# Optimization experiments

Measured on AMD Instinct MI355X. Metric: run time of the kernel, lower is better.

Reference implementation:

```python
import jax, jax.numpy as jnp
import numpy as np

N_USER = 100000
N_ITEM = 50000
N = N_USER + N_ITEM
N_EDGES = 1200000
D = 64
NEG_SLOPE = 0.01  # torch leaky_relu default
EPS = 1e-12       # torch F.normalize default


def setup_inputs() -> dict:
    key = jax.random.key(0)
    ks = jax.random.split(key, 9)
    user_emb = jax.random.normal(ks[0], (N_USER, D), dtype=jnp.float32) * 0.1
    item_emb = jax.random.normal(ks[1], (N_ITEM, D), dtype=jnp.float32) * 0.1
    edge_row = jax.random.randint(ks[2], (N_EDGES,), 0, N, dtype=jnp.int32)
    edge_col = jax.random.randint(ks[3], (N_EDGES,), 0, N, dtype=jnp.int32)
    edge_val = jax.random.uniform(ks[4], (N_EDGES,), dtype=jnp.float32)
    Wf = jax.random.normal(ks[5], (3, D, D), dtype=jnp.float32) * (1.0 / np.sqrt(D))
    bf = jnp.zeros((3, D), dtype=jnp.float32)
    Wb = jax.random.normal(ks[6], (3, D, D), dtype=jnp.float32) * (1.0 / np.sqrt(D))
    bb = jnp.zeros((3, D), dtype=jnp.float32)
    return {"user_emb": user_emb, "item_emb": item_emb,
            "edge_row": edge_row, "edge_col": edge_col, "edge_val": edge_val,
            "Wf": Wf, "bf": bf, "Wb": Wb, "bb": bb}


def _spmm_plus_eye(edge_row, edge_col, edge_val, E):
    # (H + I) @ E : gather source features, scale, segment-sum into rows, add E
    msgs = edge_val[:, None] * E[edge_col]          # [n_edges, D]
    agg = jax.ops.segment_sum(msgs, edge_row, num_segments=N)
    return agg + E


def reference(user_emb, item_emb, edge_row, edge_col, edge_val, Wf, bf, Wb, bb):
    E_l = jnp.concatenate([user_emb, item_emb], axis=0)  # [N, D]
    all_emb = [E_l]
    for i in range(3):
        front = _spmm_plus_eye(edge_row, edge_col, edge_val, E_l)
        front_cal = jax.nn.leaky_relu(front @ Wf[i].T + bf[i], NEG_SLOPE)
        back = jax.nn.leaky_relu((E_l * front) @ Wb[i].T + bb[i], NEG_SLOPE)
        E_l = front_cal + back  # dropout p=0.5 treated as eval-mode identity
        norm = jnp.maximum(jnp.linalg.norm(E_l, axis=1, keepdims=True), EPS)
        all_emb.append(E_l / norm)
    all_emb = jnp.concatenate(all_emb, axis=1)  # [N, 4*D]
    return all_emb[:N_USER], all_emb[N_USER:]
```

## Files before the change

### kernel.cpp

```cpp
#include <hip/hip_runtime.h>
#include <hip/hip_bf16.h>
#include <stdint.h>

#define N_USER 100000
#define N_ITEM 50000
#define NTOT   150000
#define NEDGE  1200000
#define D      64
#define OUTD   256
#define NEG    0.01f
#define NBLK   586
#define WPLANE 1028

__global__ void k_init(const float* __restrict__ ue, const float* __restrict__ ie,
                       float* __restrict__ E, float* __restrict__ out) {
    int t = blockIdx.x * blockDim.x + threadIdx.x;
    if (t >= NTOT * 16) return;
    int r = t >> 4, q = t & 15;
    const float* src = (r < N_USER) ? (ue + (size_t)r * D)
                                    : (ie + (size_t)(r - N_USER) * D);
    float4 v = *(const float4*)(src + q * 4);
    *(float4*)(E + (size_t)r * D + q * 4) = v;
    *(float4*)(out + (size_t)r * OUTD + q * 4) = v;
}

__global__ void k_hist(const int* __restrict__ row, int* __restrict__ cnt) {
    int e = blockIdx.x * blockDim.x + threadIdx.x;
    if (e < NEDGE) atomicAdd(&cnt[row[e]], 1);
}

__global__ void k_scan_a(const int* __restrict__ cnt, int* __restrict__ part) {
    __shared__ int s[4];
    int i = blockIdx.x * 256 + threadIdx.x;
    int v = (i < NTOT) ? cnt[i] : 0;
    for (int off = 32; off; off >>= 1) v += __shfl_down(v, off, 64);
    if ((threadIdx.x & 63) == 0) s[threadIdx.x >> 6] = v;
    __syncthreads();
    if (threadIdx.x == 0) part[blockIdx.x] = s[0] + s[1] + s[2] + s[3];
}

__global__ void k_scan_b(int* __restrict__ part) {
    __shared__ int s[1024];
    int t = threadIdx.x;
    int v = (t < NBLK) ? part[t] : 0;
    s[t] = v;
    __syncthreads();
    for (int off = 1; off < 1024; off <<= 1) {
        int x = (t >= off) ? s[t - off] : 0;
        __syncthreads();
        s[t] += x;
        __syncthreads();
    }
    if (t < NBLK) part[t] = s[t] - v;
}

__global__ void k_scan_c(const int* __restrict__ cnt, const int* __restrict__ part,
                         int* __restrict__ offs, int* __restrict__ cur) {
    __shared__ int ws[4];
    int i = blockIdx.x * 256 + threadIdx.x;
    int v = (i < NTOT) ? cnt[i] : 0;
    int lane = threadIdx.x & 63, w = threadIdx.x >> 6;
    int x = v;
    for (int o = 1; o < 64; o <<= 1) {
        int y = __shfl_up(x, o, 64);
        if (lane >= o) x += y;
    }
    if (lane == 63) ws[w] = x;
    __syncthreads();
    int base = part[blockIdx.x];
    for (int k = 0; k < w; k++) base += ws[k];
    int excl = base + x - v;
    if (i < NTOT) { offs[i] = excl; cur[i] = excl; }
    if (i == 0) offs[NTOT] = NEDGE;
}

__global__ void k_scatter(const int* __restrict__ row, const int* __restrict__ col,
                          const float* __restrict__ val, int* __restrict__ cur,
                          int2* __restrict__ ce) {
    int e = blockIdx.x * blockDim.x + threadIdx.x;
    if (e >= NEDGE) return;
    int r = row[e];
    int p = atomicAdd(&cur[r], 1);
    int2 u;
    u.x = col[e];
    u.y = __float_as_int(val[e]);
    ce[p] = u;
}

__global__ void k_spmm(const float* __restrict__ E, const int* __restrict__ offs,
                       const int2* __restrict__ ce, float* __restrict__ front) {
    int r = blockIdx.x * (blockDim.x >> 6) + (threadIdx.x >> 6);
    int d = threadIdx.x & 63;
    if (r >= NTOT) return;
    int s = offs[r], e = offs[r + 1];
    float acc = E[(size_t)r * D + d];
    float a0 = 0.f, a1 = 0.f, a2 = 0.f, a3 = 0.f;
    int p = s;
    for (; p + 4 <= e; p += 4) {
        int2 c0 = ce[p + 0];
        int2 c1 = ce[p + 1];
        int2 c2 = ce[p + 2];
        int2 c3 = ce[p + 3];
        float x0 = E[(size_t)c0.x * D + d];
        float x1 = E[(size_t)c1.x * D + d];
        float x2 = E[(size_t)c2.x * D + d];
        float x3 = E[(size_t)c3.x * D + d];
        a0 = fmaf(__int_as_float(c0.y), x0, a0);
        a1 = fmaf(__int_as_float(c1.y), x1, a1);
        a2 = fmaf(__int_as_float(c2.y), x2, a2);
        a3 = fmaf(__int_as_float(c3.y), x3, a3);
    }
    for (; p < e; ++p) {
        int2 c = ce[p];
        acc = fmaf(__int_as_float(c.y), E[(size_t)c.x * D + d], acc);
    }
    acc += (a0 + a1) + (a2 + a3);
    front[(size_t)r * D + d] = acc;
}

__global__ __launch_bounds__(256) void k_rowmv(
    const float* __restrict__ front, float* __restrict__ E,
    const float* __restrict__ Wf, const float* __restrict__ bfv,
    const float* __restrict__ Wb, const float* __restrict__ bbv,
    float* __restrict__ out, int chunk) {
    __shared__ float wfs[4 * WPLANE];
    __shared__ float wbs[4 * WPLANE];
    {
        int t  = threadIdx.x;
        int j  = t >> 2;
        int kq = t & 3;
        const float* fsrc = Wf + (size_t)j * D + kq * 16;
        const float* bsrc = Wb + (size_t)j * D + kq * 16;
        float* fdst = wfs + kq * WPLANE + j * 16;
        float* bdst = wbs + kq * WPLANE + j * 16;
        #pragma unroll
        for (int i = 0; i < 4; i++) {
            *(float4*)(fdst + i * 4) = *(const float4*)(fsrc + i * 4);
            *(float4*)(bdst + i * 4) = *(const float4*)(bsrc + i * 4);
        }
    }
    __syncthreads();

    int lane = threadIdx.x & 63;
    int w    = threadIdx.x >> 6;
    int q    = lane & 3;
    int g    = lane >> 2;
    int r    = blockIdx.x * 64 + w * 16 + g;
    if (r >= NTOT) return;

    float f[16], gg[16];
    const float* fp = front + (size_t)r * D + q * 16;
    const float* ep = E     + (size_t)r * D + q * 16;
    #pragma unroll
    for (int i = 0; i < 4; i++) {
        float4 a = *(const float4*)(fp + i * 4);
        float4 b = *(const float4*)(ep + i * 4);
        f[i*4+0] = a.x; f[i*4+1] = a.y; f[i*4+2] = a.z; f[i*4+3] = a.w;
        gg[i*4+0] = a.x*b.x; gg[i*4+1] = a.y*b.y; gg[i*4+2] = a.z*b.z; gg[i*4+3] = a.w*b.w;
    }

    const float* wfq = wfs + q * WPLANE;
    const float* wbq = wbs + q * WPLANE;

    float nsq = 0.f;
    float* erow = E + (size_t)r * D;
    #pragma unroll 1
    for (int j4 = 0; j4 < 16; j4++) {
        float e4[4];
        #pragma unroll
        for (int jj = 0; jj < 4; jj++) {
            int j = j4 * 4 + jj;
            const float* wf = wfq + j * 16;
            const float* wb = wbq + j * 16;
            float aF = 0.f, aB = 0.f;
            #pragma unroll
            for (int i = 0; i < 4; i++) {
                float4 wv = *(const float4*)(wf + i * 4);
                aF = fmaf(wv.x, f[i*4+0], aF);
                aF = fmaf(wv.y, f[i*4+1], aF);
                aF = fmaf(wv.z, f[i*4+2], aF);
                aF = fmaf(wv.w, f[i*4+3], aF);
                float4 bv = *(const float4*)(wb + i * 4);
                aB = fmaf(bv.x, gg[i*4+0], aB);
                aB = fmaf(bv.y, gg[i*4+1], aB);
                aB = fmaf(bv.z, gg[i*4+2], aB);
                aB = fmaf(bv.w, gg[i*4+3], aB);
            }
            aF += __shfl_xor(aF, 1, 64);
            aF += __shfl_xor(aF, 2, 64);
            aB += __shfl_xor(aB, 1, 64);
            aB += __shfl_xor(aB, 2, 64);
            aF += bfv[j];
            aB += bbv[j];
            float vF = (aF > 0.f) ? aF : NEG * aF;
            float vB = (aB > 0.f) ? aB : NEG * aB;
            float e = vF + vB;
            e4[jj] = e;
            nsq += e * e;
        }
        if (q == 0) {
            float4 u;
            u.x = e4[0]; u.y = e4[1]; u.z = e4[2]; u.w = e4[3];
            *(float4*)(erow + j4 * 4) = u;
        }
    }

    float inv = 1.0f / fmaxf(sqrtf(nsq), 1e-12f);
    float* orow = out + (size_t)r * OUTD + (size_t)chunk * D;
    #pragma unroll
    for (int i = 0; i < 4; i++) {
        float4 u = *(const float4*)(erow + q * 16 + i * 4);
        float4 o;
        o.x = u.x * inv; o.y = u.y * inv; o.z = u.z * inv; o.w = u.w * inv;
        *(float4*)(orow + q * 16 + i * 4) = o;
    }
}

extern "C" void kernel_launch(void* const* d_in, const int* in_sizes, int n_in,
                              void* d_out, int out_size, void* d_ws, size_t ws_size,
                              hipStream_t stream) {
    const float* ue   = (const float*)d_in[0];
    const float* ie   = (const float*)d_in[1];
    const int*   erow = (const int*)d_in[2];
    const int*   ecol = (const int*)d_in[3];
    const float* eval = (const float*)d_in[4];
    const float* Wf   = (const float*)d_in[5];
    const float* bfv  = (const float*)d_in[6];
    const float* Wb   = (const float*)d_in[7];
    const float* bbv  = (const float*)d_in[8];
    float* out = (float*)d_out;

    float* E     = (float*)d_ws;
    float* front = E + (size_t)NTOT * D;
    float* invn  = front + (size_t)NTOT * D;
    int*   cnt   = (int*)(invn + NTOT);
    int*   offs  = cnt + NTOT;
    int*   cur   = offs + NTOT + 1;
    int*   part  = cur + NTOT;
    int2*  ce    = (int2*)(part + 1024);

    hipMemsetAsync(cnt, 0, NTOT * sizeof(int), stream);
    k_init<<<(NTOT * 16 + 255) / 256, 256, 0, stream>>>(ue, ie, E, out);
    k_hist<<<(NEDGE + 255) / 256, 256, 0, stream>>>(erow, cnt);
    k_scan_a<<<NBLK, 256, 0, stream>>>(cnt, part);
    k_scan_b<<<1, 1024, 0, stream>>>(part);
    k_scan_c<<<NBLK, 256, 0, stream>>>(cnt, part, offs, cur);
    k_scatter<<<(NEDGE + 255) / 256, 256, 0, stream>>>(erow, ecol, eval, cur, ce);

    for (int i = 0; i < 3; i++) {
        k_spmm<<<(NTOT + 3) / 4, 256, 0, stream>>>(E, offs, ce, front);
        k_rowmv<<<(NTOT + 63) / 64, 256, 0, stream>>>(
            front, E, Wf + (size_t)i * D * D, bfv + (size_t)i * D,
            Wb + (size_t)i * D * D, bbv + (size_t)i * D, out, i + 1);
    }
}
```

Measured before the change: 831.7 us.

## Compute dense row transforms with split-bf16 MFMA instead of scalar FMAs

Rewrites the per-row dense transform kernel so each block handles 16 rows and computes both 64x64 matmuls with bf16 MFMA instructions. Three-term hi/lo bf16 splitting approximates fp32 accuracy. Rows are staged in LDS, and the row norm is reduced across waves through shared memory. This removes the scalar FMA loop and weight staging. The cost is per-block weight splitting work and a small precision change.

```diff
diff --git a/kernel.cpp b/kernel.cpp
--- a/kernel.cpp
+++ b/kernel.cpp
@@ -10,7 +10,33 @@
 #define OUTD   256
 #define NEG    0.01f
 #define NBLK   586
-#define WPLANE 1028
+#define LSTR   65
+
+typedef __attribute__((ext_vector_type(8))) short short8;
+typedef __attribute__((ext_vector_type(4))) float f32x4;
+
+__device__ inline ushort f2bf(float x) {
+    uint32_t u = __float_as_uint(x);
+    u += 0x7fffu + ((u >> 16) & 1u);
+    return (ushort)(u >> 16);
+}
+__device__ inline void split2(float x, ushort& h, ushort& l) {
+    ushort hh = f2bf(x);
+    float hf = __uint_as_float(((uint32_t)hh) << 16);
+    h = hh;
+    l = f2bf(x - hf);
+}
+__device__ inline void split8(const float* p, short8& h8, short8& l8) {
+    float4 v0 = *(const float4*)p;
+    float4 v1 = *(const float4*)(p + 4);
+    float vv[8] = {v0.x, v0.y, v0.z, v0.w, v1.x, v1.y, v1.z, v1.w};
+    #pragma unroll
+    for (int e = 0; e < 8; e++) {
+        ushort h, l;
+        split2(vv[e], h, l);
+        h8[e] = (short)h; l8[e] = (short)l;
+    }
+}
 
 __global__ void k_init(const float* __restrict__ ue, const float* __restrict__ ie,
                        float* __restrict__ E, float* __restrict__ out) {
@@ -123,96 +149,92 @@
     const float* __restrict__ Wf, const float* __restrict__ bfv,
     const float* __restrict__ Wb, const float* __restrict__ bbv,
     float* __restrict__ out, int chunk) {
-    __shared__ float wfs[4 * WPLANE];
-    __shared__ float wbs[4 * WPLANE];
+    __shared__ float sf[16 * LSTR];
+    __shared__ float sg[16 * LSTR];
+    __shared__ float nrm[16][4];
+
+    int t  = threadIdx.x;
+    int r0 = blockIdx.x * 16;
+
     {
-        int t  = threadIdx.x;
-        int j  = t >> 2;
-        int kq = t & 3;
-        const float* fsrc = Wf + (size_t)j * D + kq * 16;
-        const float* bsrc = Wb + (size_t)j * D + kq * 16;
-        float* fdst = wfs + kq * WPLANE + j * 16;
-        float* bdst = wbs + kq * WPLANE + j * 16;
+        int row = t >> 4, km = (t & 15) * 4;
+        const float* fp = front + (size_t)(r0 + row) * D + km;
+        const float* ep = E     + (size_t)(r0 + row) * D + km;
+        float4 a = *(const float4*)fp;
+        float4 b = *(const float4*)ep;
+        *(float4*)(sf + row * LSTR + km) = a;
+        float4 gv;
+        gv.x = a.x * b.x; gv.y = a.y * b.y; gv.z = a.z * b.z; gv.w = a.w * b.w;
+        *(float4*)(sg + row * LSTR + km) = gv;
+    }
+
+    int lane = t & 63;
+    int w    = t >> 6;
+    int cl   = lane & 15;
+    int kg   = lane >> 4;
+
+    int col = w * 16 + cl;
+
+    short8 wfh0, wfl0, wbh0, wbl0, wfh1, wfl1, wbh1, wbl1;
+    split8(Wf + (size_t)col * D +  0 + kg * 8, wfh0, wfl0);
+    split8(Wb + (size_t)col * D +  0 + kg * 8, wbh0, wbl0);
+    split8(Wf + (size_t)col * D + 32 + kg * 8, wfh1, wfl1);
+    split8(Wb + (size_t)col * D + 32 + kg * 8, wbh1, wbl1);
+    float bF = bfv[col], bB = bbv[col];
+
+    __syncthreads();
+
+    f32x4 accF = {0.f, 0.f, 0.f, 0.f};
+    f32x4 accB = {0.f, 0.f, 0.f, 0.f};
+    {
+        short8 fh, fl, gh, gl;
+        split8(sf + cl * LSTR +  0 + kg * 8, fh, fl);
+        split8(sg + cl * LSTR +  0 + kg * 8, gh, gl);
+        accF = __builtin_amdgcn_mfma_f32_16x16x32_bf16(fh, wfh0, accF, 0, 0, 0);
+        accB = __builtin_amdgcn_mfma_f32_16x16x32_bf16(gh, wbh0, accB, 0, 0, 0);
+        accF = __builtin_amdgcn_mfma_f32_16x16x32_bf16(fl, wfh0, accF, 0, 0, 0);
+        accB = __builtin_amdgcn_mfma_f32_16x16x32_bf16(gl, wbh0, accB, 0, 0, 0);
+        accF = __builtin_amdgcn_mfma_f32_16x16x32_bf16(fh, wfl0, accF, 0, 0, 0);
+        accB = __builtin_amdgcn_mfma_f32_16x16x32_bf16(gh, wbl0, accB, 0, 0, 0);
+        split8(sf + cl * LSTR + 32 + kg * 8, fh, fl);
+        split8(sg + cl * LSTR + 32 + kg * 8, gh, gl);
+        accF = __builtin_amdgcn_mfma_f32_16x16x32_bf16(fh, wfh1, accF, 0, 0, 0);
+        accB = __builtin_amdgcn_mfma_f32_16x16x32_bf16(gh, wbh1, accB, 0, 0, 0);
+        accF = __builtin_amdgcn_mfma_f32_16x16x32_bf16(fl, wfh1, accF, 0, 0, 0);
+        accB = __builtin_amdgcn_mfma_f32_16x16x32_bf16(gl, wbh1, accB, 0, 0, 0);
+        accF = __builtin_amdgcn_mfma_f32_16x16x32_bf16(fh, wfl1, accF, 0, 0, 0);
+        accB = __builtin_amdgcn_mfma_f32_16x16x32_bf16(gh, wbl1, accB, 0, 0, 0);
+    }
+
+    float e4[4], p4[4];
+    #pragma unroll
+    for (int rg = 0; rg < 4; rg++) {
+        float aF = accF[rg] + bF;
+        float aB = accB[rg] + bB;
+        float vF = (aF > 0.f) ? aF : NEG * aF;
+        float vB = (aB > 0.f) ? aB : NEG * aB;
+        float e = vF + vB;
+        e4[rg] = e;
+        float p = e * e;
+        p += __shfl_xor(p, 1, 64);
+        p += __shfl_xor(p, 2, 64);
+        p += __shfl_xor(p, 4, 64);
+        p += __shfl_xor(p, 8, 64);
+        p4[rg] = p;
+    }
+    if (cl == 0) {
         #pragma unroll
-        for (int i = 0; i < 4; i++) {
-            *(float4*)(fdst + i * 4) = *(const float4*)(fsrc + i * 4);
-            *(float4*)(bdst + i * 4) = *(const float4*)(bsrc + i * 4);
-        }
-    }
-    __syncthreads();
-
-    int lane = threadIdx.x & 63;
-    int w    = threadIdx.x >> 6;
-    int q    = lane & 3;
-    int g    = lane >> 2;
-    int r    = blockIdx.x * 64 + w * 16 + g;
-    if (r >= NTOT) return;
-
-    float f[16], gg[16];
-    const float* fp = front + (size_t)r * D + q * 16;
-    const float* ep = E     + (size_t)r * D + q * 16;
+        for (int rg = 0; rg < 4; rg++) nrm[kg * 4 + rg][w] = p4[rg];
+    }
+    __syncthreads();
     #pragma unroll
-    for (int i = 0; i < 4; i++) {
-        float4 a = *(const float4*)(fp + i * 4);
-        float4 b = *(const float4*)(ep + i * 4);
-        f[i*4+0] = a.x; f[i*4+1] = a.y; f[i*4+2] = a.z; f[i*4+3] = a.w;
-        gg[i*4+0] = a.x*b.x; gg[i*4+1] = a.y*b.y; gg[i*4+2] = a.z*b.z; gg[i*4+3] = a.w*b.w;
-    }
-
-    const float* wfq = wfs + q * WPLANE;
-    const float* wbq = wbs + q * WPLANE;
-
-    float nsq = 0.f;
-    float* erow = E + (size_t)r * D;
-    #pragma unroll 1
-    for (int j4 = 0; j4 < 16; j4++) {
-        float e4[4];
-        #pragma unroll
-        for (int jj = 0; jj < 4; jj++) {
-            int j = j4 * 4 + jj;
-            const float* wf = wfq + j * 16;
-            const float* wb = wbq + j * 16;
-            float aF = 0.f, aB = 0.f;
-            #pragma unroll
-            for (int i = 0; i < 4; i++) {
-                float4 wv = *(const float4*)(wf + i * 4);
-                aF = fmaf(wv.x, f[i*4+0], aF);
-                aF = fmaf(wv.y, f[i*4+1], aF);
-                aF = fmaf(wv.z, f[i*4+2], aF);
-                aF = fmaf(wv.w, f[i*4+3], aF);
-                float4 bv = *(const float4*)(wb + i * 4);
-                aB = fmaf(bv.x, gg[i*4+0], aB);
-                aB = fmaf(bv.y, gg[i*4+1], aB);
-                aB = fmaf(bv.z, gg[i*4+2], aB);
-                aB = fmaf(bv.w, gg[i*4+3], aB);
-            }
-            aF += __shfl_xor(aF, 1, 64);
-            aF += __shfl_xor(aF, 2, 64);
-            aB += __shfl_xor(aB, 1, 64);
-            aB += __shfl_xor(aB, 2, 64);
-            aF += bfv[j];
-            aB += bbv[j];
-            float vF = (aF > 0.f) ? aF : NEG * aF;
-            float vB = (aB > 0.f) ? aB : NEG * aB;
-            float e = vF + vB;
-            e4[jj] = e;
-            nsq += e * e;
-        }
-        if (q == 0) {
-            float4 u;
-            u.x = e4[0]; u.y = e4[1]; u.z = e4[2]; u.w = e4[3];
-            *(float4*)(erow + j4 * 4) = u;
-        }
-    }
-
-    float inv = 1.0f / fmaxf(sqrtf(nsq), 1e-12f);
-    float* orow = out + (size_t)r * OUTD + (size_t)chunk * D;
-    #pragma unroll
-    for (int i = 0; i < 4; i++) {
-        float4 u = *(const float4*)(erow + q * 16 + i * 4);
-        float4 o;
-        o.x = u.x * inv; o.y = u.y * inv; o.z = u.z * inv; o.w = u.w * inv;
-        *(float4*)(orow + q * 16 + i * 4) = o;
+    for (int rg = 0; rg < 4; rg++) {
+        int row = kg * 4 + rg;
+        float4 nv = *(const float4*)&nrm[row][0];
+        float nsq = (nv.x + nv.y) + (nv.z + nv.w);
+        float inv = 1.0f / fmaxf(sqrtf(nsq), 1e-12f);
+        E[(size_t)(r0 + row) * D + col] = e4[rg];
+        out[(size_t)(r0 + row) * OUTD + (size_t)chunk * D + col] = e4[rg] * inv;
     }
 }
 
@@ -249,7 +271,7 @@
 
     for (int i = 0; i < 3; i++) {
         k_spmm<<<(NTOT + 3) / 4, 256, 0, stream>>>(E, offs, ce, front);
-        k_rowmv<<<(NTOT + 63) / 64, 256, 0, stream>>>(
+        k_rowmv<<<NTOT / 16, 256, 0, stream>>>(
             front, E, Wf + (size_t)i * D * D, bfv + (size_t)i * D,
             Wb + (size_t)i * D * D, bbv + (size_t)i * D, out, i + 1);
     }
```

Result: faster. 700.7 us (-15.8%).
